# Kernel tuning notes

Hardware: AMD Instinct MI355X
Metric: run time of the kernel (lower is better)

Reference implementation:

```python
import jax, jax.numpy as jnp
import numpy as np

DIM = 1024
NUM_HEADS = 16
HEAD_DIM = DIM // NUM_HEADS
SCALE = HEAD_DIM ** -0.5
CAUSAL = True


def setup_inputs() -> dict:
    key = jax.random.key(0)
    k_x, k_qkv, k_proj, k_pb = jax.random.split(key, 4)
    B, S = 4, 2048
    x = jax.random.normal(k_x, (B, S, DIM), dtype=jnp.float32)
    # nn.Linear(dim, 3*dim, bias=False): weight [3*dim, dim]; store transposed [dim, 3*dim]
    w_qkv = jax.random.normal(k_qkv, (DIM, 3 * DIM), dtype=jnp.float32) * (DIM ** -0.5)
    w_proj = jax.random.normal(k_proj, (DIM, DIM), dtype=jnp.float32) * (DIM ** -0.5)
    b_proj = jax.random.normal(k_pb, (DIM,), dtype=jnp.float32) * 0.01
    return {"x": x, "w_qkv": w_qkv, "w_proj": w_proj, "b_proj": b_proj}


def reference(x, w_qkv, w_proj, b_proj):
    B, S, C = x.shape
    # qkv: [B, S, 3, H, D] -> q,k,v each [B, H, S, D]
    qkv = (x @ w_qkv).reshape(B, S, 3, NUM_HEADS, HEAD_DIM)
    qkv = jnp.transpose(qkv, (2, 0, 3, 1, 4))
    q, k, v = qkv[0], qkv[1], qkv[2]
    # scores [B, H, S, S]
    attn = jnp.einsum('bhqd,bhkd->bhqk', q, k) * SCALE
    if CAUSAL:
        causal_mask = jnp.triu(jnp.ones((S, S), dtype=bool), k=1)
        attn = jnp.where(causal_mask, -jnp.inf, attn)
    attn = jax.nn.softmax(attn, axis=-1)
    out = jnp.einsum('bhqk,bhkd->bhqd', attn, v)
    out = jnp.transpose(out, (0, 2, 1, 3)).reshape(B, S, C)
    return out @ w_proj + b_proj
```

## Files before the change

### kernel.cpp

```cpp
#include <hip/hip_runtime.h>
#include <hip/hip_bf16.h>
#include <math.h>

#define DIMC 1024
#define NHEADS 16
#define HDIM 64
#define BATCH 4
#define SEQ 2048
#define NROWS (BATCH * SEQ)
#define ATTN_SCALE 0.125f
#define LOG2E 1.4426950408889634f

typedef __attribute__((ext_vector_type(8))) short short8;
typedef __attribute__((ext_vector_type(4))) short short4v;
typedef __attribute__((ext_vector_type(4))) float f32x4;

static __device__ __forceinline__ short f2bf(float f) {
    __hip_bfloat16 h = __float2bfloat16(f);
    return *reinterpret_cast<short*>(&h);
}

static __device__ __forceinline__ void gload16(const void* g, void* l) {
    __builtin_amdgcn_global_load_lds(
        (const __attribute__((address_space(1))) unsigned int*)g,
        (__attribute__((address_space(3))) unsigned int*)l, 16, 0, 0);
}

__global__ __launch_bounds__(256)
void xcvt(const float* __restrict__ in, unsigned short* __restrict__ out) {
    int i = blockIdx.x * 256 + threadIdx.x;
    const float4* p = reinterpret_cast<const float4*>(in) + 2 * i;
    float4 a = p[0], b = p[1];
    short8 pk;
    pk[0] = f2bf(a.x); pk[1] = f2bf(a.y); pk[2] = f2bf(a.z); pk[3] = f2bf(a.w);
    pk[4] = f2bf(b.x); pk[5] = f2bf(b.y); pk[6] = f2bf(b.z); pk[7] = f2bf(b.w);
    reinterpret_cast<short8*>(out)[i] = pk;
}

__global__ __launch_bounds__(256)
void transpose_cvt(const float* __restrict__ src, unsigned short* __restrict__ dst,
                   int N) {
    __shared__ float t[64][65];
    const int tid = threadIdx.x;
    const int cb = blockIdx.x * 64;
    const int rb = blockIdx.y * 64;
#pragma unroll
    for (int e = 0; e < 4; e++) {
        int idx = tid + e * 256;
        int row = idx >> 4;
        int c4 = (idx & 15) << 2;
        *reinterpret_cast<float4*>(&t[row][c4]) =
            *reinterpret_cast<const float4*>(&src[(size_t)(rb + row) * N + cb + c4]);
    }
    __syncthreads();
#pragma unroll
    for (int e = 0; e < 2; e++) {
        int idx = tid + e * 256;
        int col = idx >> 3;
        int k8 = (idx & 7) << 3;
        short8 pk;
#pragma unroll
        for (int j = 0; j < 8; j++) pk[j] = f2bf(t[k8 + j][col]);
        *reinterpret_cast<short8*>(&dst[(size_t)(cb + col) * 1024 + rb + k8]) = pk;
    }
}

__global__ __launch_bounds__(256)
void qkv_gemm_mfma(const unsigned short* __restrict__ Xbf,
                   const unsigned short* __restrict__ Wt,
                   unsigned short* __restrict__ qo, unsigned short* __restrict__ ko,
                   unsigned short* __restrict__ vt) {
    __shared__ short Alds[128][64];
    __shared__ short Blds[128][64];
    const int tid = threadIdx.x;
    const int lane = tid & 63;
    const int wave = tid >> 6;
    const int wr = wave >> 1, wc = wave & 1;
    const int rowbase = blockIdx.y * 128;
    const int colbase = blockIdx.x * 128;
    const int g = lane >> 4, li = lane & 15;
    const int sr = lane >> 3;
    const int sc = ((lane & 7) ^ sr) * 8;
    const int swk = li & 7;
    short* aflat = &Alds[0][0];
    short* bflat = &Blds[0][0];

    f32x4 acc[4][4];
#pragma unroll
    for (int m = 0; m < 4; m++)
#pragma unroll
        for (int n = 0; n < 4; n++) acc[m][n] = (f32x4){0.f, 0.f, 0.f, 0.f};

    for (int k0 = 0; k0 < DIMC; k0 += 64) {
#pragma unroll
        for (int e = 0; e < 4; e++) {
            int j = wave * 4 + e;
            gload16(&Xbf[(size_t)(rowbase + j * 8 + sr) * DIMC + k0 + sc],
                    aflat + j * 512);
            gload16(&Wt[(size_t)(colbase + j * 8 + sr) * 1024 + k0 + sc],
                    bflat + j * 512);
        }
        __syncthreads();
#pragma unroll
        for (int ks = 0; ks < 2; ks++) {
            short8 af[4], bfr[4];
#pragma unroll
            for (int m = 0; m < 4; m++)
                af[m] = *reinterpret_cast<const short8*>(
                    &Alds[wr * 64 + m * 16 + li][((ks * 4 + g) ^ swk) * 8]);
#pragma unroll
            for (int n = 0; n < 4; n++)
                bfr[n] = *reinterpret_cast<const short8*>(
                    &Blds[wc * 64 + n * 16 + li][((ks * 4 + g) ^ swk) * 8]);
#pragma unroll
            for (int m = 0; m < 4; m++)
#pragma unroll
                for (int n = 0; n < 4; n++)
                    acc[m][n] = __builtin_amdgcn_mfma_f32_16x16x32_bf16(
                        af[m], bfr[n], acc[m][n], 0, 0, 0);
        }
        __syncthreads();
    }

    const int col0 = colbase + wc * 64;
    const int three = col0 >> 10;
    const int h = (col0 & 1023) >> 6;
    if (three < 2) {
        unsigned short* dst = (three == 0) ? qo : ko;
        const float mult = (three == 0) ? (ATTN_SCALE * LOG2E) : 1.0f;
#pragma unroll
        for (int n = 0; n < 4; n++) {
            int d = n * 16 + li;
#pragma unroll
            for (int m = 0; m < 4; m++) {
                int r0 = rowbase + wr * 64 + m * 16 + g * 4;
                int b = r0 >> 11;
                size_t base = ((size_t)(b * NHEADS + h) * SEQ) * HDIM + d;
#pragma unroll
                for (int r = 0; r < 4; r++) {
                    int s = (r0 + r) & 2047;
                    dst[base + (size_t)s * HDIM] = (unsigned short)f2bf(acc[m][n][r] * mult);
                }
            }
        }
    } else {
#pragma unroll
        for (int n = 0; n < 4; n++) {
            int d = n * 16 + li;
#pragma unroll
            for (int m = 0; m < 4; m++) {
                int r0 = rowbase + wr * 64 + m * 16 + g * 4;
                int b = r0 >> 11, s0 = r0 & 2047;
                short4v pk;
#pragma unroll
                for (int r = 0; r < 4; r++) pk[r] = f2bf(acc[m][n][r]);
                *reinterpret_cast<short4v*>(
                    &vt[((size_t)(b * NHEADS + h) * HDIM + d) * SEQ + s0]) = pk;
            }
        }
    }
}

__global__ __launch_bounds__(256)
void proj_gemm_mfma(const unsigned short* __restrict__ Abf,
                    const unsigned short* __restrict__ Wt,
                    const float* __restrict__ bias, float* __restrict__ out) {
    __shared__ short Alds[128][64];
    __shared__ short Blds[128][64];
    const int tid = threadIdx.x;
    const int lane = tid & 63;
    const int wave = tid >> 6;
    const int wr = wave >> 1, wc = wave & 1;
    const int rowbase = blockIdx.y * 128;
    const int colbase = blockIdx.x * 128;
    const int g = lane >> 4, li = lane & 15;
    const int sr = lane >> 3;
    const int sc = ((lane & 7) ^ sr) * 8;
    const int swk = li & 7;
    short* aflat = &Alds[0][0];
    short* bflat = &Blds[0][0];

    f32x4 acc[4][4];
#pragma unroll
    for (int m = 0; m < 4; m++)
#pragma unroll
        for (int n = 0; n < 4; n++) acc[m][n] = (f32x4){0.f, 0.f, 0.f, 0.f};

    for (int k0 = 0; k0 < DIMC; k0 += 64) {
#pragma unroll
        for (int e = 0; e < 4; e++) {
            int j = wave * 4 + e;
            gload16(&Abf[(size_t)(rowbase + j * 8 + sr) * DIMC + k0 + sc],
                    aflat + j * 512);
            gload16(&Wt[(size_t)(colbase + j * 8 + sr) * 1024 + k0 + sc],
                    bflat + j * 512);
        }
        __syncthreads();
#pragma unroll
        for (int ks = 0; ks < 2; ks++) {
            short8 af[4], bfr[4];
#pragma unroll
            for (int m = 0; m < 4; m++)
                af[m] = *reinterpret_cast<const short8*>(
                    &Alds[wr * 64 + m * 16 + li][((ks * 4 + g) ^ swk) * 8]);
#pragma unroll
            for (int n = 0; n < 4; n++)
                bfr[n] = *reinterpret_cast<const short8*>(
                    &Blds[wc * 64 + n * 16 + li][((ks * 4 + g) ^ swk) * 8]);
#pragma unroll
            for (int m = 0; m < 4; m++)
#pragma unroll
                for (int n = 0; n < 4; n++)
                    acc[m][n] = __builtin_amdgcn_mfma_f32_16x16x32_bf16(
                        af[m], bfr[n], acc[m][n], 0, 0, 0);
        }
        __syncthreads();
    }

#pragma unroll
    for (int n = 0; n < 4; n++) {
        int col = colbase + wc * 64 + n * 16 + li;
        float bv = bias[col];
#pragma unroll
        for (int m = 0; m < 4; m++) {
            int r0 = rowbase + wr * 64 + m * 16 + g * 4;
#pragma unroll
            for (int r = 0; r < 4; r++)
                out[(size_t)(r0 + r) * DIMC + col] = acc[m][n][r] + bv;
        }
    }
}

__global__ __launch_bounds__(512)
void flash_attn_mfma(const unsigned short* __restrict__ qg,
                     const unsigned short* __restrict__ kg,
                     const unsigned short* __restrict__ vt,
                     unsigned short* __restrict__ og) {
    __shared__ short Klds[2][64][64];
    __shared__ short Vlds[2][64][64];
    __shared__ short Plds[8][16][64];
    const int tid = threadIdx.x;
    const int lane = tid & 63;
    const int w = tid >> 6;
    const int g = lane >> 4, li = lane & 15;
    const int sw = li & 7;
    const int orig = blockIdx.x;
    const int swz = (orig & 7) * 64 + (orig >> 3);
    const int bx = swz & 7;
    const int bh = swz >> 3;
    const size_t head = (size_t)bh * SEQ * HDIM;
    const int b = bh >> 4, h = bh & 15;

    const int c0r = tid >> 3, c0c = tid & 7;

    for (int pass = 0; pass < 2; pass++) {
        const int qtile = pass ? (15 - bx) : bx;
        const int qbase = qtile * 128;
        const int qw = qbase + w * 16;
        const int nt = 2 * qtile + 2;

        short8 bq[2];
#pragma unroll
        for (int ds = 0; ds < 2; ds++)
            bq[ds] = *reinterpret_cast<const short8*>(
                &qg[head + (size_t)(qw + li) * HDIM + ds * 32 + g * 8]);

        f32x4 accO[4];
#pragma unroll
        for (int df = 0; df < 4; df++) accO[df] = (f32x4){0.f, 0.f, 0.f, 0.f};
        float mrow = -INFINITY;
        float lrow = 0.f;

        const unsigned short* kp = kg + head + (size_t)c0r * HDIM + c0c * 8;
        const unsigned short* vp = vt + head + (size_t)c0r * SEQ + c0c * 8;

        short8 kreg, vreg;
        kreg = *reinterpret_cast<const short8*>(kp);
        vreg = *reinterpret_cast<const short8*>(vp);
        kp += 64 * HDIM; vp += 64;
        {
            const int sw0 = (c0c ^ (c0r & 7)) * 8;
            *reinterpret_cast<short8*>(&Klds[0][c0r][sw0]) = kreg;
            *reinterpret_cast<short8*>(&Vlds[0][c0r][sw0]) = vreg;
        }
        __syncthreads();

        for (int t = 0; t < nt; t++) {
            const int kvbase = t * 64;
            const int buf = t & 1;
            const bool more = (t + 1 < nt);
            if (more) {
                kreg = *reinterpret_cast<const short8*>(kp);
                vreg = *reinterpret_cast<const short8*>(vp);
                kp += 64 * HDIM; vp += 64;
            }

            if (kvbase <= qw + 15) {
                f32x4 s[4];
#pragma unroll
                for (int m = 0; m < 4; m++) s[m] = (f32x4){0.f, 0.f, 0.f, 0.f};
#pragma unroll
                for (int ds = 0; ds < 2; ds++) {
                    short8 ak[4];
#pragma unroll
                    for (int m = 0; m < 4; m++)
                        ak[m] = *reinterpret_cast<const short8*>(
                            &Klds[buf][li + 16 * m][((ds * 4 + g) ^ sw) * 8]);
#pragma unroll
                    for (int m = 0; m < 4; m++)
                        s[m] = __builtin_amdgcn_mfma_f32_16x16x32_bf16(
                            ak[m], bq[ds], s[m], 0, 0, 0);
                }
                const bool diag = (kvbase + 63 > qw);
                if (diag) {
                    int q = qw + li;
#pragma unroll
                    for (int m = 0; m < 4; m++)
#pragma unroll
                        for (int r = 0; r < 4; r++) {
                            int kv = kvbase + 16 * m + 4 * g + r;
                            if (kv > q) s[m][r] = -INFINITY;
                        }
                }
                float a0 = fmaxf(fmaxf(s[0][0], s[0][1]), fmaxf(s[0][2], s[0][3]));
                float a1 = fmaxf(fmaxf(s[1][0], s[1][1]), fmaxf(s[1][2], s[1][3]));
                float a2 = fmaxf(fmaxf(s[2][0], s[2][1]), fmaxf(s[2][2], s[2][3]));
                float a3 = fmaxf(fmaxf(s[3][0], s[3][1]), fmaxf(s[3][2], s[3][3]));
                float tm = fmaxf(fmaxf(a0, a1), fmaxf(a2, a3));
                tm = fmaxf(tm, __shfl_xor(tm, 16));
                tm = fmaxf(tm, __shfl_xor(tm, 32));
                float mnew = fmaxf(mrow, tm);
                float corr = __builtin_amdgcn_exp2f(mrow - mnew);
                mrow = mnew;
                float sm[4];
#pragma unroll
                for (int m = 0; m < 4; m++) {
                    float p0 = __builtin_amdgcn_exp2f(s[m][0] - mrow);
                    float p1 = __builtin_amdgcn_exp2f(s[m][1] - mrow);
                    float p2 = __builtin_amdgcn_exp2f(s[m][2] - mrow);
                    float p3 = __builtin_amdgcn_exp2f(s[m][3] - mrow);
                    sm[m] = (p0 + p1) + (p2 + p3);
                    unsigned u01 = (__float_as_uint(p1) & 0xFFFF0000u) |
                                   (__float_as_uint(p0) >> 16);
                    unsigned u23 = (__float_as_uint(p3) & 0xFFFF0000u) |
                                   (__float_as_uint(p2) >> 16);
                    *reinterpret_cast<uint2*>(
                        &Plds[w][li][((2 * m + (g >> 1)) ^ sw) * 8 + (g & 1) * 4]) =
                        make_uint2(u01, u23);
                }
                float ts = (sm[0] + sm[1]) + (sm[2] + sm[3]);
                ts += __shfl_xor(ts, 16);
                ts += __shfl_xor(ts, 32);
                lrow = lrow * corr + ts;
                if (!__all((int)(corr == 1.0f))) {
#pragma unroll
                    for (int df = 0; df < 4; df++) {
                        accO[df][0] *= corr; accO[df][1] *= corr;
                        accO[df][2] *= corr; accO[df][3] *= corr;
                    }
                }
#pragma unroll
                for (int ks = 0; ks < 2; ks++) {
                    short8 av[4];
#pragma unroll
                    for (int df = 0; df < 4; df++)
                        av[df] = *reinterpret_cast<const short8*>(
                            &Vlds[buf][li + 16 * df][((ks * 4 + g) ^ sw) * 8]);
                    short8 bp = *reinterpret_cast<const short8*>(
                        &Plds[w][li][((ks * 4 + g) ^ sw) * 8]);
#pragma unroll
                    for (int df = 0; df < 4; df++)
                        accO[df] = __builtin_amdgcn_mfma_f32_16x16x32_bf16(
                            av[df], bp, accO[df], 0, 0, 0);
                }
            }

            if (more) {
                const int nbuf = buf ^ 1;
                const int sw0 = (c0c ^ (c0r & 7)) * 8;
                *reinterpret_cast<short8*>(&Klds[nbuf][c0r][sw0]) = kreg;
                *reinterpret_cast<short8*>(&Vlds[nbuf][c0r][sw0]) = vreg;
            }
            __syncthreads();
        }

        {
            float inv = 1.0f / lrow;
            int q = qw + li;
            size_t rowoff = (size_t)(b * SEQ + q) * DIMC + h * HDIM;
#pragma unroll
            for (int df = 0; df < 4; df++) {
                short4v pk;
#pragma unroll
                for (int r = 0; r < 4; r++) pk[r] = f2bf(accO[df][r] * inv);
                *reinterpret_cast<short4v*>(&og[rowoff + 16 * df + 4 * g]) = pk;
            }
        }
        __syncthreads();
    }
}

extern "C" void kernel_launch(void* const* d_in, const int* in_sizes, int n_in,
                              void* d_out, int out_size, void* d_ws, size_t ws_size,
                              hipStream_t stream) {
    const float* x      = (const float*)d_in[0];
    const float* w_qkv  = (const float*)d_in[1];
    const float* w_proj = (const float*)d_in[2];
    const float* b_proj = (const float*)d_in[3];
    float* out = (float*)d_out;

    char* w = (char*)d_ws;
    unsigned short* qb  = (unsigned short*)(w);
    unsigned short* kb  = (unsigned short*)(w + ((size_t)16 << 20));
    unsigned short* vtb = (unsigned short*)(w + ((size_t)32 << 20));
    unsigned short* ao  = (unsigned short*)(w + ((size_t)48 << 20));
    unsigned short* wqt = (unsigned short*)(w + ((size_t)64 << 20));
    unsigned short* wpt = (unsigned short*)(w + ((size_t)72 << 20));
    unsigned short* xbf = (unsigned short*)(w + ((size_t)80 << 20));

    xcvt<<<NROWS * DIMC / (256 * 8), 256, 0, stream>>>(x, xbf);
    transpose_cvt<<<dim3(3 * DIMC / 64, DIMC / 64), 256, 0, stream>>>(w_qkv, wqt, 3 * DIMC);
    transpose_cvt<<<dim3(DIMC / 64, DIMC / 64), 256, 0, stream>>>(w_proj, wpt, DIMC);
    qkv_gemm_mfma<<<dim3(3 * DIMC / 128, NROWS / 128), 256, 0, stream>>>(xbf, wqt, qb, kb, vtb);
    flash_attn_mfma<<<512, 512, 0, stream>>>(qb, kb, vtb, ao);
    proj_gemm_mfma<<<dim3(DIMC / 128, NROWS / 128), 256, 0, stream>>>(ao, wpt, b_proj, out);
}
```

Baseline: 250.7 us.

## Keep softmax probabilities in registers by permuting K rows to match MFMA layout

The K rows loaded for the QK^T MFMA are permuted so that the score accumulator layout directly matches the B-operand layout needed for the PV MFMA. The P tile can then be packed into bf16 registers instead of going through a per-wave LDS round trip, which removes the LDS writes and reads for P. The causal mask indices are recomputed for the permuted layout, and s_setprio is placed around the MFMA groups to favour matrix issue. The risk is higher register pressure and a subtle layout mistake that would silently corrupt the output.

Measured after the change: 247.6 us. No clear change (-1.2%).

```diff
diff --git a/kernel.cpp b/kernel.cpp
--- a/kernel.cpp
+++ b/kernel.cpp
@@ -238,12 +238,10 @@
                      unsigned short* __restrict__ og) {
     __shared__ short Klds[2][64][64];
     __shared__ short Vlds[2][64][64];
-    __shared__ short Plds[8][16][64];
     const int tid = threadIdx.x;
     const int lane = tid & 63;
     const int w = tid >> 6;
     const int g = lane >> 4, li = lane & 15;
-    const int sw = li & 7;
     const int orig = blockIdx.x;
     const int swz = (orig & 7) * 64 + (orig >> 3);
     const int bx = swz & 7;
@@ -252,6 +250,9 @@
     const int b = bh >> 4, h = bh & 15;
 
     const int c0r = tid >> 3, c0c = tid & 7;
+
+    const int abase0 = 8 * (li >> 2) + (li & 3);
+    const int abase1 = abase0 + 4;
 
     for (int pass = 0; pass < 2; pass++) {
         const int qtile = pass ? (15 - bx) : bx;
@@ -303,24 +304,28 @@
                 for (int ds = 0; ds < 2; ds++) {
                     short8 ak[4];
 #pragma unroll
-                    for (int m = 0; m < 4; m++)
+                    for (int m = 0; m < 4; m++) {
+                        int arow = 32 * (m >> 1) + ((m & 1) ? abase1 : abase0);
                         ak[m] = *reinterpret_cast<const short8*>(
-                            &Klds[buf][li + 16 * m][((ds * 4 + g) ^ sw) * 8]);
+                            &Klds[buf][arow][((ds * 4 + g) ^ (arow & 7)) * 8]);
+                    }
+                    __builtin_amdgcn_s_setprio(1);
 #pragma unroll
                     for (int m = 0; m < 4; m++)
                         s[m] = __builtin_amdgcn_mfma_f32_16x16x32_bf16(
                             ak[m], bq[ds], s[m], 0, 0, 0);
+                    __builtin_amdgcn_s_setprio(0);
                 }
                 const bool diag = (kvbase + 63 > qw);
                 if (diag) {
                     int q = qw + li;
 #pragma unroll
-                    for (int m = 0; m < 4; m++)
-#pragma unroll
-                        for (int r = 0; r < 4; r++) {
-                            int kv = kvbase + 16 * m + 4 * g + r;
-                            if (kv > q) s[m][r] = -INFINITY;
-                        }
+                    for (int m = 0; m < 4; m++) {
+                        int kv0 = kvbase + 32 * (m >> 1) + 8 * g + 4 * (m & 1);
+#pragma unroll
+                        for (int r = 0; r < 4; r++)
+                            if (kv0 + r > q) s[m][r] = -INFINITY;
+                    }
                 }
                 float a0 = fmaxf(fmaxf(s[0][0], s[0][1]), fmaxf(s[0][2], s[0][3]));
                 float a1 = fmaxf(fmaxf(s[1][0], s[1][1]), fmaxf(s[1][2], s[1][3]));
@@ -332,21 +337,28 @@
                 float mnew = fmaxf(mrow, tm);
                 float corr = __builtin_amdgcn_exp2f(mrow - mnew);
                 mrow = mnew;
+                float p[4][4];
                 float sm[4];
 #pragma unroll
                 for (int m = 0; m < 4; m++) {
-                    float p0 = __builtin_amdgcn_exp2f(s[m][0] - mrow);
-                    float p1 = __builtin_amdgcn_exp2f(s[m][1] - mrow);
-                    float p2 = __builtin_amdgcn_exp2f(s[m][2] - mrow);
-                    float p3 = __builtin_amdgcn_exp2f(s[m][3] - mrow);
-                    sm[m] = (p0 + p1) + (p2 + p3);
-                    unsigned u01 = (__float_as_uint(p1) & 0xFFFF0000u) |
-                                   (__float_as_uint(p0) >> 16);
-                    unsigned u23 = (__float_as_uint(p3) & 0xFFFF0000u) |
-                                   (__float_as_uint(p2) >> 16);
-                    *reinterpret_cast<uint2*>(
-                        &Plds[w][li][((2 * m + (g >> 1)) ^ sw) * 8 + (g & 1) * 4]) =
-                        make_uint2(u01, u23);
+#pragma unroll
+                    for (int r = 0; r < 4; r++)
+                        p[m][r] = __builtin_amdgcn_exp2f(s[m][r] - mrow);
+                    sm[m] = (p[m][0] + p[m][1]) + (p[m][2] + p[m][3]);
+                }
+                short8 bp[2];
+#pragma unroll
+                for (int ks = 0; ks < 2; ks++) {
+                    unsigned u0 = (__float_as_uint(p[2 * ks][1]) & 0xFFFF0000u) |
+                                  (__float_as_uint(p[2 * ks][0]) >> 16);
+                    unsigned u1 = (__float_as_uint(p[2 * ks][3]) & 0xFFFF0000u) |
+                                  (__float_as_uint(p[2 * ks][2]) >> 16);
+                    unsigned u2 = (__float_as_uint(p[2 * ks + 1][1]) & 0xFFFF0000u) |
+                                  (__float_as_uint(p[2 * ks + 1][0]) >> 16);
+                    unsigned u3 = (__float_as_uint(p[2 * ks + 1][3]) & 0xFFFF0000u) |
+                                  (__float_as_uint(p[2 * ks + 1][2]) >> 16);
+                    unsigned q4[4] = {u0, u1, u2, u3};
+                    bp[ks] = *reinterpret_cast<short8*>(q4);
                 }
                 float ts = (sm[0] + sm[1]) + (sm[2] + sm[3]);
                 ts += __shfl_xor(ts, 16);
@@ -363,15 +375,17 @@
                 for (int ks = 0; ks < 2; ks++) {
                     short8 av[4];
 #pragma unroll
-                    for (int df = 0; df < 4; df++)
+                    for (int df = 0; df < 4; df++) {
+                        int vrow = li + 16 * df;
                         av[df] = *reinterpret_cast<const short8*>(
-                            &Vlds[buf][li + 16 * df][((ks * 4 + g) ^ sw) * 8]);
-                    short8 bp = *reinterpret_cast<const short8*>(
-                        &Plds[w][li][((ks * 4 + g) ^ sw) * 8]);
+                            &Vlds[buf][vrow][((ks * 4 + g) ^ (vrow & 7)) * 8]);
+                    }
+                    __builtin_amdgcn_s_setprio(1);
 #pragma unroll
                     for (int df = 0; df < 4; df++)
                         accO[df] = __builtin_amdgcn_mfma_f32_16x16x32_bf16(
-                            av[df], bp, accO[df], 0, 0, 0);
+                            av[df], bp[ks], accO[df], 0, 0, 0);
+                    __builtin_amdgcn_s_setprio(0);
                 }
             }
 
```
